# Optimization experiments

Measured on AMD Instinct MI355X. Metric: run time of the kernel, lower is better.

Reference implementation:

```python
import jax, jax.numpy as jnp
import numpy as np

N_HEAD = 16
LN_EPS = 1e-5

def _layernorm(x, g, b):
    mu = jnp.mean(x, axis=-1, keepdims=True)
    var = jnp.mean(jnp.square(x - mu), axis=-1, keepdims=True)
    return (x - mu) * jax.lax.rsqrt(var + LN_EPS) * g + b

def setup_inputs() -> dict:
    key = jax.random.key(0)
    ks = jax.random.split(key, 8)
    B, T, C, L, V = 4, 512, 1024, 8, 32000
    s = 0.02
    return {
        "idx": jax.random.randint(ks[0], (B, T), 0, V, dtype=jnp.int32),
        "tok_emb": jax.random.normal(ks[1], (V, C), jnp.float32) * s,
        "pos_emb": jax.random.normal(ks[2], (T, C), jnp.float32) * s,
        "ln1_g": jnp.ones((L, C), jnp.float32),
        "ln1_b": jnp.zeros((L, C), jnp.float32),
        "attn_w": jax.random.normal(ks[3], (L, 3 * C, C), jnp.float32) * s,
        "proj_w": jax.random.normal(ks[4], (L, C, C), jnp.float32) * s,
        "ln2_g": jnp.ones((L, C), jnp.float32),
        "ln2_b": jnp.zeros((L, C), jnp.float32),
        "mlp_w1": jax.random.normal(ks[5], (L, 4 * C, C), jnp.float32) * s,
        "mlp_w2": jax.random.normal(ks[6], (L, C, 4 * C), jnp.float32) * s,
        "lnf_g": jnp.ones((C,), jnp.float32),
        "lnf_b": jnp.zeros((C,), jnp.float32),
        "head_w": jax.random.normal(ks[7], (V, C), jnp.float32) * s,
    }

def reference(idx, tok_emb, pos_emb, ln1_g, ln1_b, attn_w, proj_w,
              ln2_g, ln2_b, mlp_w1, mlp_w2, lnf_g, lnf_b, head_w):
    B, T = idx.shape
    C = tok_emb.shape[1]
    H = N_HEAD
    D = C // H
    scale = 1.0 / np.sqrt(D).astype(np.float32)
    x = tok_emb[idx] + pos_emb[:T]            # [B,T,C]
    causal = jnp.tril(jnp.ones((T, T), bool))  # [T,T]

    def block(x, p):
        g1, b1, wqkv, wp, g2, b2, w1, w2 = p
        h = _layernorm(x, g1, b1)
        qkv = h @ wqkv.T                       # [B,T,3C]
        q, k, v = jnp.split(qkv, 3, axis=-1)
        q = q.reshape(B, T, H, D).transpose(0, 2, 1, 3)  # [B,H,T,D]
        k = k.reshape(B, T, H, D).transpose(0, 2, 1, 3)
        v = v.reshape(B, T, H, D).transpose(0, 2, 1, 3)
        att = jnp.einsum('bhqd,bhkd->bhqk', q, k) * scale
        att = jnp.where(causal, att, -jnp.inf)
        att = jax.nn.softmax(att, axis=-1)
        y = jnp.einsum('bhqk,bhkd->bhqd', att, v)
        y = y.transpose(0, 2, 1, 3).reshape(B, T, C)
        a = x + y @ wp.T                       # attn residual (inner)
        m = jax.nn.gelu(_layernorm(a, g2, b2) @ w1.T, approximate=False) @ w2.T
        # NOTE: faithful to source: outer residual adds x, not a
        return x + m, None

    x, _ = jax.lax.scan(block, x, (ln1_g, ln1_b, attn_w, proj_w,
                                   ln2_g, ln2_b, mlp_w1, mlp_w2))
    x = _layernorm(x, lnf_g, lnf_b)
    logits = x @ head_w.T                      # [B,T,V]
    return logits
```

## Files before the change

kernel.cpp:

```cpp
#include <hip/hip_runtime.h>
#include <stdint.h>

typedef unsigned short u16;
typedef __bf16 bf16_t;
typedef bf16_t bf16x8 __attribute__((ext_vector_type(8)));
typedef float f32x4 __attribute__((ext_vector_type(4)));

static __device__ __forceinline__ u16 f2bf(float f) {
  union { float f; uint32_t u; } cv; cv.f = f;
  uint32_t u = cv.u;
  return (u16)((u + 0x7FFFu + ((u >> 16) & 1u)) >> 16);
}

static __device__ __forceinline__ void gload16(const void* g, void* l) {
  __builtin_amdgcn_global_load_lds(
      (__attribute__((address_space(1))) void*)g,
      (__attribute__((address_space(3))) void*)l, 16, 0, 0);
}

__global__ __launch_bounds__(256) void embed_kernel(const int* __restrict__ idx,
                                                    const float* __restrict__ tok,
                                                    const float* __restrict__ pos,
                                                    float* __restrict__ x) {
  int row = blockIdx.x, tid = threadIdx.x;
  int t = row & 511;
  int v = idx[row];
  float4 a = ((const float4*)(tok + (long)v * 1024))[tid];
  float4 p = ((const float4*)(pos + (long)t * 1024))[tid];
  a.x += p.x; a.y += p.y; a.z += p.z; a.w += p.w;
  ((float4*)(x + (long)row * 1024))[tid] = a;
}

__global__ __launch_bounds__(256) void ln_kernel(const float* __restrict__ in,
                                                 const float* __restrict__ g,
                                                 const float* __restrict__ b,
                                                 u16* __restrict__ out) {
  int row = blockIdx.x, tid = threadIdx.x;
  int wid = tid >> 6, lane = tid & 63;
  const float4 v = ((const float4*)(in + (long)row * 1024))[tid];
  float s1 = v.x + v.y + v.z + v.w;
  float s2 = v.x*v.x + v.y*v.y + v.z*v.z + v.w*v.w;
#pragma unroll
  for (int o = 32; o >= 1; o >>= 1) { s1 += __shfl_xor(s1, o); s2 += __shfl_xor(s2, o); }
  __shared__ float red1[4], red2[4];
  if (lane == 0) { red1[wid] = s1; red2[wid] = s2; }
  __syncthreads();
  s1 = red1[0] + red1[1] + red1[2] + red1[3];
  s2 = red2[0] + red2[1] + red2[2] + red2[3];
  float mu = s1 * (1.f/1024.f);
  float var = s2 * (1.f/1024.f) - mu*mu;
  float rstd = rsqrtf(var + 1e-5f);
  const float4 gg = ((const float4*)g)[tid];
  const float4 bb = ((const float4*)b)[tid];
  ushort4 o4;
  o4.x = f2bf((v.x - mu)*rstd*gg.x + bb.x);
  o4.y = f2bf((v.y - mu)*rstd*gg.y + bb.y);
  o4.z = f2bf((v.z - mu)*rstd*gg.z + bb.z);
  o4.w = f2bf((v.w - mu)*rstd*gg.w + bb.w);
  ((ushort4*)(out + (long)row * 1024))[tid] = o4;
}

__global__ __launch_bounds__(256) void cast_kernel(const float* __restrict__ src,
                                                   u16* __restrict__ dst, int n4) {
  int i = blockIdx.x * 256 + threadIdx.x;
  if (i >= n4) return;
  float4 v = ((const float4*)src)[i];
  ushort4 o; o.x = f2bf(v.x); o.y = f2bf(v.y); o.z = f2bf(v.z); o.w = f2bf(v.w);
  ((ushort4*)dst)[i] = o;
}

__global__ __launch_bounds__(256) void cast4_kernel(const float* __restrict__ s0,
                                                    const float* __restrict__ s1,
                                                    const float* __restrict__ s2,
                                                    const float* __restrict__ s3,
                                                    u16* __restrict__ d0, u16* __restrict__ d1,
                                                    u16* __restrict__ d2, u16* __restrict__ d3) {
  int i = blockIdx.x * 256 + threadIdx.x;
  const float* s; u16* d; int off;
  if (i < 786432)       { s = s0; d = d0; off = i; }
  else if (i < 1048576) { s = s1; d = d1; off = i - 786432; }
  else if (i < 2097152) { s = s2; d = d2; off = i - 1048576; }
  else                  { s = s3; d = d3; off = i - 2097152; }
  float4 v = ((const float4*)s)[off];
  ushort4 o; o.x = f2bf(v.x); o.y = f2bf(v.y); o.z = f2bf(v.z); o.w = f2bf(v.w);
  ((ushort4*)d)[off] = o;
}

__global__ __launch_bounds__(256) void softmax_kernel(const float* __restrict__ S,
                                                      u16* __restrict__ P) {
  int wid = threadIdx.x >> 6, lane = threadIdx.x & 63;
  long R = (long)blockIdx.x * 4 + wid;
  int q = (int)(R & 511);
  const float* row = S + R * 512;
  float v[8];
  float m = -3.4e38f;
#pragma unroll
  for (int j = 0; j < 8; ++j) {
    int t = j*64 + lane;
    v[j] = (t <= q) ? row[t] : -3.4e38f;
    m = fmaxf(m, v[j]);
  }
#pragma unroll
  for (int o = 32; o >= 1; o >>= 1) m = fmaxf(m, __shfl_xor(m, o));
  float s = 0.f;
#pragma unroll
  for (int j = 0; j < 8; ++j) {
    int t = j*64 + lane;
    v[j] = (t <= q) ? __expf(v[j] - m) : 0.f;
    s += v[j];
  }
#pragma unroll
  for (int o = 32; o >= 1; o >>= 1) s += __shfl_xor(s, o);
  float inv = 1.f / s;
  u16* prow = P + R * 512;
#pragma unroll
  for (int j = 0; j < 8; ++j) prow[j*64 + lane] = f2bf(v[j] * inv);
}

enum { EPI_F32 = 0, EPI_BF16 = 1, EPI_RES = 2, EPI_GELU = 3, EPI_QKV = 4 };

template<int BN, int EPI, bool CSKIP, bool CKLIM>
__global__ __launch_bounds__(256, 2) void gemm_nt(
    const u16* __restrict__ A, const u16* __restrict__ Bw,
    float* __restrict__ Cf, u16* __restrict__ Cb, const float* __restrict__ Res,
    int K, int ldc, float scale,
    long sAz, long sBz, long sCb, long sCh, int Hdiv,
    u16* __restrict__ q_out, u16* __restrict__ k_out, u16* __restrict__ vt_out) {
  constexpr int BM = 128, BK = 32;
  __shared__ __align__(16) u16 As[BM * BK];
  __shared__ __align__(16) u16 Bs[BN * BK];
  const int tid = threadIdx.x;
  const int wid = tid >> 6, lane = tid & 63;
  const int n0 = blockIdx.x * BN, m0 = blockIdx.y * BM;
  const long z = blockIdx.z;
  if (CSKIP && n0 > m0) return;
  const u16* Ab = A + z * sAz;
  const u16* Bb = Bw + z * sBz;
  int kend = K;
  if (CKLIM) { int ke = m0 + BM; kend = ke < K ? ke : K; }

  const int wm = wid & 1, wn = wid >> 1;
  constexpr int NF = BN / 32;
  constexpr int BPW = BN / 64;
  f32x4 acc[4][NF];
  f32x4 zero = {0.f, 0.f, 0.f, 0.f};
#pragma unroll
  for (int i = 0; i < 4; ++i)
#pragma unroll
    for (int j = 0; j < NF; ++j) acc[i][j] = zero;

  const int fA0 = (wid * 2) * 64 + lane, fA1 = fA0 + 64;
  const u16* gA0 = Ab + (long)(m0 + (fA0 >> 2)) * K + ((fA0 & 3) << 3);
  const u16* gA1 = Ab + (long)(m0 + (fA1 >> 2)) * K + ((fA1 & 3) << 3);
  u16* lA0 = &As[(wid * 2) * 512];
  u16* lA1 = lA0 + 512;
  const u16* gB[BPW]; u16* lB[BPW];
#pragma unroll
  for (int i = 0; i < BPW; ++i) {
    int f = (wid * BPW + i) * 64 + lane;
    gB[i] = Bb + (long)(n0 + (f >> 2)) * K + ((f & 3) << 3);
    lB[i] = &Bs[(wid * BPW + i) * 512];
  }
  const int lm = lane & 15, lq = lane >> 4;

  for (int k0 = 0; k0 < kend; k0 += BK) {
    __syncthreads();
    gload16(gA0 + k0, lA0);
    gload16(gA1 + k0, lA1);
#pragma unroll
    for (int i = 0; i < BPW; ++i) gload16(gB[i] + k0, lB[i]);
    __syncthreads();
    bf16x8 af[4], bfr[NF];
#pragma unroll
    for (int i = 0; i < 4; ++i)
      af[i] = *(const bf16x8*)&As[(wm * 64 + i * 16 + lm) * BK + lq * 8];
#pragma unroll
    for (int j = 0; j < NF; ++j)
      bfr[j] = *(const bf16x8*)&Bs[(wn * (BN / 2) + j * 16 + lm) * BK + lq * 8];
#pragma unroll
    for (int i = 0; i < 4; ++i)
#pragma unroll
      for (int j = 0; j < NF; ++j)
        acc[i][j] = __builtin_amdgcn_mfma_f32_16x16x32_bf16(af[i], bfr[j], acc[i][j], 0, 0, 0);
  }

  const long coff = (z / Hdiv) * sCb + (z % Hdiv) * sCh;
#pragma unroll
  for (int i = 0; i < 4; ++i) {
#pragma unroll
    for (int j = 0; j < NF; ++j) {
#pragma unroll
      for (int r = 0; r < 4; ++r) {
        int row = m0 + wm * 64 + i * 16 + lq * 4 + r;
        int col = n0 + wn * (BN / 2) + j * 16 + lm;
        float v = acc[i][j][r];
        if (EPI == EPI_F32) {
          Cf[coff + (long)row * ldc + col] = v * scale;
        } else if (EPI == EPI_BF16) {
          Cb[coff + (long)row * ldc + col] = f2bf(v);
        } else if (EPI == EPI_RES) {
          long idx = (long)row * ldc + col;
          Cf[idx] = Res[idx] + v;
        } else if (EPI == EPI_GELU) {
          float gl = 0.5f * v * (1.0f + erff(v * 0.70710678118654752f));
          Cb[(long)row * ldc + col] = f2bf(gl);
        } else {
          int which = col >> 10, wc = col & 1023;
          int hh = wc >> 6, d = wc & 63;
          int bb2 = row >> 9, t = row & 511;
          long bh = bb2 * 16 + hh;
          u16 val = f2bf(v);
          if (which == 0)      q_out[(bh * 512 + t) * 64 + d] = val;
          else if (which == 1) k_out[(bh * 512 + t) * 64 + d] = val;
          else                 vt_out[(bh * 64 + d) * 512 + t] = val;
        }
      }
    }
  }
}

extern "C" void kernel_launch(void* const* d_in, const int* in_sizes, int n_in,
                              void* d_out, int out_size, void* d_ws, size_t ws_size,
                              hipStream_t stream) {
  (void)in_sizes; (void)n_in; (void)out_size; (void)ws_size;
  const int*   idx   = (const int*)  d_in[0];
  const float* tok   = (const float*)d_in[1];
  const float* pos   = (const float*)d_in[2];
  const float* ln1g  = (const float*)d_in[3];
  const float* ln1b  = (const float*)d_in[4];
  const float* attnw = (const float*)d_in[5];
  const float* projw = (const float*)d_in[6];
  const float* ln2g  = (const float*)d_in[7];
  const float* ln2b  = (const float*)d_in[8];
  const float* w1w   = (const float*)d_in[9];
  const float* w2w   = (const float*)d_in[10];
  const float* lnfg  = (const float*)d_in[11];
  const float* lnfb  = (const float*)d_in[12];
  const float* headw = (const float*)d_in[13];

  char* ob = (char*)d_out;
  float* Sf  = (float*)(ob + 0);
  u16*   Pb  = (u16*)  (ob + 67108864);
  u16*   m1b = (u16*)  (ob + 100663296);
  u16*   Qb  = (u16*)  (ob + 117440512);
  u16*   Kb  = (u16*)  (ob + 121634816);
  u16*   Vtb = (u16*)  (ob + 125829120);
  u16*   yb  = (u16*)  (ob + 130023424);
  float* ab  = (float*)(ob + 134217728);
  float* xb  = (float*)(ob + 142606336);

  char* wsb = (char*)d_ws;
  u16* hb    = (u16*)(wsb + 0);
  u16* wqkvb = (u16*)(wsb + 4194304);
  u16* wpb   = (u16*)(wsb + 10485760);
  u16* w1b   = (u16*)(wsb + 12582912);
  u16* w2b   = (u16*)(wsb + 20971520);
  u16* headb = (u16*)(wsb + 29360128);

  embed_kernel<<<2048, 256, 0, stream>>>(idx, tok, pos, xb);

  for (int l = 0; l < 8; ++l) {
    cast4_kernel<<<12288, 256, 0, stream>>>(
        attnw + (size_t)l * 3145728, projw + (size_t)l * 1048576,
        w1w + (size_t)l * 4194304,   w2w + (size_t)l * 4194304,
        wqkvb, wpb, w1b, w2b);
    ln_kernel<<<2048, 256, 0, stream>>>(xb, ln1g + l * 1024, ln1b + l * 1024, hb);
    gemm_nt<128, EPI_QKV, false, false><<<dim3(24, 16, 1), 256, 0, stream>>>(
        hb, wqkvb, nullptr, nullptr, nullptr, 1024, 0, 1.f,
        0, 0, 0, 0, 1, Qb, Kb, Vtb);
    gemm_nt<128, EPI_F32, true, false><<<dim3(4, 4, 64), 256, 0, stream>>>(
        Qb, Kb, Sf, nullptr, nullptr, 64, 512, 0.125f,
        32768, 32768, 262144, 0, 1, nullptr, nullptr, nullptr);
    softmax_kernel<<<8192, 256, 0, stream>>>(Sf, Pb);
    gemm_nt<64, EPI_BF16, false, true><<<dim3(1, 4, 64), 256, 0, stream>>>(
        Pb, Vtb, nullptr, yb, nullptr, 512, 1024, 1.f,
        262144, 32768, 524288, 64, 16, nullptr, nullptr, nullptr);
    gemm_nt<128, EPI_RES, false, false><<<dim3(8, 16, 1), 256, 0, stream>>>(
        yb, wpb, ab, nullptr, xb, 1024, 1024, 1.f,
        0, 0, 0, 0, 1, nullptr, nullptr, nullptr);
    ln_kernel<<<2048, 256, 0, stream>>>(ab, ln2g + l * 1024, ln2b + l * 1024, hb);
    gemm_nt<128, EPI_GELU, false, false><<<dim3(32, 16, 1), 256, 0, stream>>>(
        hb, w1b, nullptr, m1b, nullptr, 1024, 4096, 1.f,
        0, 0, 0, 0, 1, nullptr, nullptr, nullptr);
    gemm_nt<128, EPI_RES, false, false><<<dim3(8, 16, 1), 256, 0, stream>>>(
        m1b, w2b, xb, nullptr, xb, 4096, 1024, 1.f,
        0, 0, 0, 0, 1, nullptr, nullptr, nullptr);
  }

  ln_kernel<<<2048, 256, 0, stream>>>(xb, lnfg, lnfb, hb);
  cast_kernel<<<32000, 256, 0, stream>>>(headw, headb, 8192000);
  gemm_nt<128, EPI_F32, false, false><<<dim3(250, 16, 1), 256, 0, stream>>>(
      hb, headb, (float*)d_out, nullptr, nullptr, 1024, 32000, 1.f,
      0, 0, 0, 0, 1, nullptr, nullptr, nullptr);
}
```

Before: 2.568 ms.

## Fuse QK^T with causal softmax and remap GEMM blocks for XCD locality

Replaces the separate QK^T GEMM (fp32 score matrix written to memory) and softmax kernel with one kernel that computes a 64x512 score tile per block and applies the masked softmax in registers, writing only bf16 probabilities. It also adds an XSWAP block remapping that spreads consecutive block IDs across 8 chunks, so blocks sharing A/B tiles land on the same XCD, and halves BN for the two residual GEMMs to raise block count. The fused kernel holds many accumulators per thread, which risks register pressure, and it recomputes the masked upper-triangle work instead of skipping it.

```diff
diff --git a/kernel.cpp b/kernel.cpp
--- a/kernel.cpp
+++ b/kernel.cpp
@@ -86,40 +86,129 @@
   ((ushort4*)d)[off] = o;
 }
 
-__global__ __launch_bounds__(256) void softmax_kernel(const float* __restrict__ S,
-                                                      u16* __restrict__ P) {
-  int wid = threadIdx.x >> 6, lane = threadIdx.x & 63;
-  long R = (long)blockIdx.x * 4 + wid;
-  int q = (int)(R & 511);
-  const float* row = S + R * 512;
-  float v[8];
-  float m = -3.4e38f;
-#pragma unroll
-  for (int j = 0; j < 8; ++j) {
-    int t = j*64 + lane;
-    v[j] = (t <= q) ? row[t] : -3.4e38f;
-    m = fmaxf(m, v[j]);
-  }
-#pragma unroll
-  for (int o = 32; o >= 1; o >>= 1) m = fmaxf(m, __shfl_xor(m, o));
-  float s = 0.f;
-#pragma unroll
-  for (int j = 0; j < 8; ++j) {
-    int t = j*64 + lane;
-    v[j] = (t <= q) ? __expf(v[j] - m) : 0.f;
-    s += v[j];
-  }
-#pragma unroll
-  for (int o = 32; o >= 1; o >>= 1) s += __shfl_xor(s, o);
-  float inv = 1.f / s;
-  u16* prow = P + R * 512;
-#pragma unroll
-  for (int j = 0; j < 8; ++j) prow[j*64 + lane] = f2bf(v[j] * inv);
+__global__ __launch_bounds__(256, 2) void qk_softmax_kernel(
+    const u16* __restrict__ Q, const u16* __restrict__ Kt, u16* __restrict__ P) {
+  constexpr int BK = 32;
+  __shared__ __align__(16) u16 As[64 * BK];
+  __shared__ __align__(16) u16 Bs[512 * BK];
+  __shared__ float redmx[2][64], redsm[2][64];
+  const int tid = threadIdx.x;
+  const int wid = tid >> 6, lane = tid & 63;
+  const int lm = lane & 15, lq = lane >> 4;
+  const int wm = wid & 1, wn = wid >> 1;
+  const int m0 = blockIdx.x * 64;
+  const long z = blockIdx.z;
+  const u16* Ab = Q + z * 32768;
+  const u16* Bb = Kt + z * 32768;
+
+  f32x4 acc[2][16];
+  f32x4 zero = {0.f, 0.f, 0.f, 0.f};
+#pragma unroll
+  for (int i = 0; i < 2; ++i)
+#pragma unroll
+    for (int j = 0; j < 16; ++j) acc[i][j] = zero;
+
+  const int fA = wid * 64 + lane;
+  const u16* gA = Ab + (long)(m0 + (fA >> 2)) * 64 + ((fA & 3) << 3);
+  u16* lA = &As[wid * 512];
+  const u16* gB[8]; u16* lB[8];
+#pragma unroll
+  for (int i = 0; i < 8; ++i) {
+    int f = (wid * 8 + i) * 64 + lane;
+    gB[i] = Bb + (long)(f >> 2) * 64 + ((f & 3) << 3);
+    lB[i] = &Bs[(wid * 8 + i) * 512];
+  }
+
+#pragma unroll
+  for (int k0 = 0; k0 < 64; k0 += BK) {
+    __syncthreads();
+    gload16(gA + k0, lA);
+#pragma unroll
+    for (int i = 0; i < 8; ++i) gload16(gB[i] + k0, lB[i]);
+    __syncthreads();
+    bf16x8 af0 = *(const bf16x8*)&As[(wm * 32 + 0 * 16 + lm) * BK + lq * 8];
+    bf16x8 af1 = *(const bf16x8*)&As[(wm * 32 + 1 * 16 + lm) * BK + lq * 8];
+#pragma unroll
+    for (int j = 0; j < 16; ++j) {
+      bf16x8 bfr = *(const bf16x8*)&Bs[(wn * 256 + j * 16 + lm) * BK + lq * 8];
+      acc[0][j] = __builtin_amdgcn_mfma_f32_16x16x32_bf16(af0, bfr, acc[0][j], 0, 0, 0);
+      acc[1][j] = __builtin_amdgcn_mfma_f32_16x16x32_bf16(af1, bfr, acc[1][j], 0, 0, 0);
+    }
+  }
+
+  float mx[2][4];
+#pragma unroll
+  for (int i = 0; i < 2; ++i)
+#pragma unroll
+    for (int r = 0; r < 4; ++r) {
+      int q = m0 + wm * 32 + i * 16 + lq * 4 + r;
+      float m = -3.4e38f;
+#pragma unroll
+      for (int j = 0; j < 16; ++j) {
+        int col = wn * 256 + j * 16 + lm;
+        float v = (col <= q) ? acc[i][j][r] * 0.125f : -3.4e38f;
+        acc[i][j][r] = v;
+        m = fmaxf(m, v);
+      }
+#pragma unroll
+      for (int o = 8; o >= 1; o >>= 1) m = fmaxf(m, __shfl_xor(m, o));
+      mx[i][r] = m;
+    }
+  if (lm == 0) {
+#pragma unroll
+    for (int i = 0; i < 2; ++i)
+#pragma unroll
+      for (int r = 0; r < 4; ++r)
+        redmx[wn][wm * 32 + i * 16 + lq * 4 + r] = mx[i][r];
+  }
+  __syncthreads();
+
+  float sm[2][4];
+#pragma unroll
+  for (int i = 0; i < 2; ++i)
+#pragma unroll
+    for (int r = 0; r < 4; ++r) {
+      int rowloc = wm * 32 + i * 16 + lq * 4 + r;
+      float m = fmaxf(redmx[0][rowloc], redmx[1][rowloc]);
+      float s = 0.f;
+#pragma unroll
+      for (int j = 0; j < 16; ++j) {
+        float e = __expf(acc[i][j][r] - m);
+        acc[i][j][r] = e;
+        s += e;
+      }
+#pragma unroll
+      for (int o = 8; o >= 1; o >>= 1) s += __shfl_xor(s, o);
+      sm[i][r] = s;
+    }
+  if (lm == 0) {
+#pragma unroll
+    for (int i = 0; i < 2; ++i)
+#pragma unroll
+      for (int r = 0; r < 4; ++r)
+        redsm[wn][wm * 32 + i * 16 + lq * 4 + r] = sm[i][r];
+  }
+  __syncthreads();
+
+  const int wlim = (m0 & ~127) + 128;
+#pragma unroll
+  for (int i = 0; i < 2; ++i)
+#pragma unroll
+    for (int r = 0; r < 4; ++r) {
+      int rowloc = wm * 32 + i * 16 + lq * 4 + r;
+      float inv = 1.f / (redsm[0][rowloc] + redsm[1][rowloc]);
+      u16* prow = P + z * 262144 + (long)(m0 + rowloc) * 512;
+#pragma unroll
+      for (int j = 0; j < 16; ++j) {
+        int col = wn * 256 + j * 16 + lm;
+        if (col < wlim) prow[col] = f2bf(acc[i][j][r] * inv);
+      }
+    }
 }
 
 enum { EPI_F32 = 0, EPI_BF16 = 1, EPI_RES = 2, EPI_GELU = 3, EPI_QKV = 4 };
 
-template<int BN, int EPI, bool CSKIP, bool CKLIM>
+template<int BN, int EPI, bool CKLIM, bool XSWAP>
 __global__ __launch_bounds__(256, 2) void gemm_nt(
     const u16* __restrict__ A, const u16* __restrict__ Bw,
     float* __restrict__ Cf, u16* __restrict__ Cb, const float* __restrict__ Res,
@@ -131,9 +220,15 @@
   __shared__ __align__(16) u16 Bs[BN * BK];
   const int tid = threadIdx.x;
   const int wid = tid >> 6, lane = tid & 63;
-  const int n0 = blockIdx.x * BN, m0 = blockIdx.y * BM;
+  int mb, nb;
+  if (XSWAP) {
+    unsigned p = blockIdx.x + (blockIdx.y << 4);
+    unsigned chunk = (gridDim.x * gridDim.y) >> 3;
+    unsigned lg = (p & 7u) * chunk + (p >> 3);
+    mb = (int)(lg & 15u); nb = (int)(lg >> 4);
+  } else { nb = blockIdx.x; mb = blockIdx.y; }
+  const int n0 = nb * BN, m0 = mb * BM;
   const long z = blockIdx.z;
-  if (CSKIP && n0 > m0) return;
   const u16* Ab = A + z * sAz;
   const u16* Bb = Bw + z * sBz;
   int kend = K;
@@ -239,7 +334,6 @@
   const float* headw = (const float*)d_in[13];
 
   char* ob = (char*)d_out;
-  float* Sf  = (float*)(ob + 0);
   u16*   Pb  = (u16*)  (ob + 67108864);
   u16*   m1b = (u16*)  (ob + 100663296);
   u16*   Qb  = (u16*)  (ob + 117440512);
@@ -265,31 +359,28 @@
         w1w + (size_t)l * 4194304,   w2w + (size_t)l * 4194304,
         wqkvb, wpb, w1b, w2b);
     ln_kernel<<<2048, 256, 0, stream>>>(xb, ln1g + l * 1024, ln1b + l * 1024, hb);
-    gemm_nt<128, EPI_QKV, false, false><<<dim3(24, 16, 1), 256, 0, stream>>>(
+    gemm_nt<128, EPI_QKV, false, true><<<dim3(16, 24, 1), 256, 0, stream>>>(
         hb, wqkvb, nullptr, nullptr, nullptr, 1024, 0, 1.f,
         0, 0, 0, 0, 1, Qb, Kb, Vtb);
-    gemm_nt<128, EPI_F32, true, false><<<dim3(4, 4, 64), 256, 0, stream>>>(
-        Qb, Kb, Sf, nullptr, nullptr, 64, 512, 0.125f,
-        32768, 32768, 262144, 0, 1, nullptr, nullptr, nullptr);
-    softmax_kernel<<<8192, 256, 0, stream>>>(Sf, Pb);
-    gemm_nt<64, EPI_BF16, false, true><<<dim3(1, 4, 64), 256, 0, stream>>>(
+    qk_softmax_kernel<<<dim3(8, 1, 64), 256, 0, stream>>>(Qb, Kb, Pb);
+    gemm_nt<64, EPI_BF16, true, false><<<dim3(1, 4, 64), 256, 0, stream>>>(
         Pb, Vtb, nullptr, yb, nullptr, 512, 1024, 1.f,
         262144, 32768, 524288, 64, 16, nullptr, nullptr, nullptr);
-    gemm_nt<128, EPI_RES, false, false><<<dim3(8, 16, 1), 256, 0, stream>>>(
+    gemm_nt<64, EPI_RES, false, true><<<dim3(16, 16, 1), 256, 0, stream>>>(
         yb, wpb, ab, nullptr, xb, 1024, 1024, 1.f,
         0, 0, 0, 0, 1, nullptr, nullptr, nullptr);
     ln_kernel<<<2048, 256, 0, stream>>>(ab, ln2g + l * 1024, ln2b + l * 1024, hb);
-    gemm_nt<128, EPI_GELU, false, false><<<dim3(32, 16, 1), 256, 0, stream>>>(
+    gemm_nt<128, EPI_GELU, false, true><<<dim3(16, 32, 1), 256, 0, stream>>>(
         hb, w1b, nullptr, m1b, nullptr, 1024, 4096, 1.f,
         0, 0, 0, 0, 1, nullptr, nullptr, nullptr);
-    gemm_nt<128, EPI_RES, false, false><<<dim3(8, 16, 1), 256, 0, stream>>>(
+    gemm_nt<64, EPI_RES, false, true><<<dim3(16, 16, 1), 256, 0, stream>>>(
         m1b, w2b, xb, nullptr, xb, 4096, 1024, 1.f,
         0, 0, 0, 0, 1, nullptr, nullptr, nullptr);
   }
 
   ln_kernel<<<2048, 256, 0, stream>>>(xb, lnfg, lnfb, hb);
   cast_kernel<<<32000, 256, 0, stream>>>(headw, headb, 8192000);
-  gemm_nt<128, EPI_F32, false, false><<<dim3(250, 16, 1), 256, 0, stream>>>(
+  gemm_nt<128, EPI_F32, false, true><<<dim3(16, 250, 1), 256, 0, stream>>>(
       hb, headb, (float*)d_out, nullptr, nullptr, 1024, 32000, 1.f,
       0, 0, 0, 0, 1, nullptr, nullptr, nullptr);
 }
```

After: 2.393 ms. 1.07x faster.
